# Kernel optimization log

Hardware: AMD Instinct MI355X
Metric: run time of the kernel (lower is better)

Reference implementation:

```python
import jax, jax.numpy as jnp
import numpy as np

GROUP_DIMS = (128, 64, 128, 64)  # per-group feature widths, sum = 384
ATTN_OUT = 64                    # per-group attention output width
B, W = 65536, 3                  # batch, words (4 groups * 3 words * 64 = 768 = linear_inner in-features)


def setup_inputs() -> dict:
    key = jax.random.key(0)
    keys = iter(jax.random.split(key, 64))
    s = 0.02
    inp = {"words": jax.random.normal(next(keys), (B, W, sum(GROUP_DIMS)), jnp.float32)}
    for g, d in enumerate(GROUP_DIMS):
        inp[f"wqkv{g}"] = jax.random.normal(next(keys), (d, 3 * d), jnp.float32) * s
        inp[f"bqkv{g}"] = jnp.zeros((3 * d,), jnp.float32)
        inp[f"wo{g}"] = jax.random.normal(next(keys), (d, ATTN_OUT), jnp.float32) * s
        inp[f"bo{g}"] = jnp.zeros((ATTN_OUT,), jnp.float32)
    inp["wi"] = jax.random.normal(next(keys), (ATTN_OUT * 12, 256), jnp.float32) * s
    inp["bi"] = jnp.zeros((256,), jnp.float32)
    inp["wout"] = jax.random.normal(next(keys), (256, 1), jnp.float32) * s
    inp["bout"] = jnp.zeros((1,), jnp.float32)
    return inp


def _group_attn(x, wqkv, bqkv, wo, bo, d):
    # x: [B, W, d] -> self-attention over W words within this feature group
    qkv = x @ wqkv + bqkv                      # [B, W, 3d]
    q, k, v = jnp.split(qkv, 3, axis=-1)       # each [B, W, d]
    scores = jnp.einsum('bqd,bkd->bqk', q, k) / jnp.sqrt(jnp.float32(d))
    attn = jax.nn.softmax(scores, axis=-1)     # [B, W, W]
    out = jnp.einsum('bqk,bkd->bqd', attn, v)  # [B, W, d]
    return out @ wo + bo                       # [B, W, ATTN_OUT]


def reference(words, wqkv0, bqkv0, wo0, bo0, wqkv1, bqkv1, wo1, bo1,
              wqkv2, bqkv2, wo2, bo2, wqkv3, bqkv3, wo3, bo3,
              wi, bi, wout, bout):
    gp = [(wqkv0, bqkv0, wo0, bo0), (wqkv1, bqkv1, wo1, bo1),
          (wqkv2, bqkv2, wo2, bo2), (wqkv3, bqkv3, wo3, bo3)]
    outs, start = [], 0
    for (wqkv, bqkv, wo, bo), d in zip(gp, GROUP_DIMS):
        outs.append(_group_attn(words[..., start:start + d], wqkv, bqkv, wo, bo, d))
        start += d
    cat = jnp.concatenate(outs, axis=-2)                 # [B, 12, 64]
    flat = jax.nn.relu(cat.reshape(cat.shape[0], -1))    # [B, 768]
    inner = jax.nn.relu(flat @ wi + bi)                  # [B, 256]
    return inner @ wout + bout                           # [B, 1]
```

## Files before the change

### kernel.cpp

```cpp
#include <hip/hip_runtime.h>

typedef _Float16 f16;
typedef _Float16 half8 __attribute__((ext_vector_type(8)));
typedef _Float16 half4 __attribute__((ext_vector_type(4)));
typedef float f32x4 __attribute__((ext_vector_type(4)));

#define BTOT 65536

static const size_t OFF_FLAT = 0;
static const size_t SZ_FLAT  = (size_t)BTOT * 768 * 2;
static const size_t OFF_WIT  = OFF_FLAT + SZ_FLAT;
static const size_t SZ_WIT   = (size_t)256 * 768 * 2;
static const size_t SZ_WT128 = (size_t)208 * 128 * 2;
static const size_t SZ_WT64  = (size_t)144 * 64 * 2;
static const size_t OFF_WT0  = OFF_WIT + SZ_WIT;
static const size_t OFF_WT1  = OFF_WT0 + SZ_WT128;
static const size_t OFF_WT2  = OFF_WT1 + SZ_WT64;
static const size_t OFF_WT3  = OFF_WT2 + SZ_WT128;
static const size_t OFF_CO   = OFF_WT3 + SZ_WT64;
static const size_t OFF_C    = OFF_CO + 256 * 4;

__global__ __launch_bounds__(256) void pk_fuse(
    const float* __restrict__ wq0, const float* __restrict__ bq0, const float* __restrict__ wo0, const float* __restrict__ bo0,
    const float* __restrict__ wq1, const float* __restrict__ bq1, const float* __restrict__ wo1, const float* __restrict__ bo1,
    const float* __restrict__ wq2, const float* __restrict__ bq2, const float* __restrict__ wo2, const float* __restrict__ bo2,
    const float* __restrict__ wq3, const float* __restrict__ bq3, const float* __restrict__ wo3, const float* __restrict__ bo3,
    f16* __restrict__ wT0, f16* __restrict__ wT1, f16* __restrict__ wT2, f16* __restrict__ wT3,
    float* __restrict__ coAll, float* __restrict__ cAll)
{
    const int g = blockIdx.y;
    const float* wqkv; const float* bqkv; const float* wo; const float* bo; f16* wT; int D;
    switch (g) {
        case 0:  wqkv = wq0; bqkv = bq0; wo = wo0; bo = bo0; wT = wT0; D = 128; break;
        case 1:  wqkv = wq1; bqkv = bq1; wo = wo1; bo = bo1; wT = wT1; D = 64;  break;
        case 2:  wqkv = wq2; bqkv = bq2; wo = wo2; bo = bo2; wT = wT2; D = 128; break;
        default: wqkv = wq3; bqkv = bq3; wo = wo3; bo = bo3; wT = wT3; D = 64;  break;
    }
    const int sh = (D == 128) ? 7 : 6;
    const int NT = (D + 81) / 16;
    const int NTD = (NT * 16) << sh;
    const int total = NTD + 65;
    const int o = blockIdx.x * 256 + threadIdx.x;
    if (o >= total) return;
    const int s3 = 3 * D;
    const float sc = rsqrtf((float)D);
    if (o < NTD) {
        const int n = o >> sh, k = o & (D - 1);
        float val = 0.f;
        if (n < D) {
            const float* a = wqkv + (size_t)k * s3;
            const float* b = wqkv + (size_t)n * s3 + D;
            float s = 0.f;
            for (int m = 0; m < D; ++m) s += a[m] * b[m];
            val = s * sc;
        } else if (n < D + 64) {
            const int j = n - D;
            const float* a = wqkv + (size_t)k * s3 + 2 * D;
            float s = 0.f;
            for (int m = 0; m < D; ++m) s += a[m] * wo[m * 64 + j];
            val = s;
        } else if (n == D + 64) {
            const float* a = wqkv + (size_t)k * s3;
            float s = 0.f;
            for (int m = 0; m < D; ++m) s += a[m] * bqkv[D + m];
            val = s * sc;
        } else if (n == D + 65) {
            const float* a = wqkv + (size_t)k * s3 + D;
            float s = 0.f;
            for (int m = 0; m < D; ++m) s += a[m] * bqkv[m];
            val = s * sc;
        }
        wT[o] = (f16)val;
    } else if (o < NTD + 64) {
        const int j = o - NTD;
        float s = 0.f;
        for (int m = 0; m < D; ++m) s += bqkv[2 * D + m] * wo[m * 64 + j];
        coAll[g * 64 + j] = s + bo[j];
    } else {
        float s = 0.f;
        for (int m = 0; m < D; ++m) s += bqkv[m] * bqkv[D + m];
        cAll[g] = s * sc;
    }
}

__global__ __launch_bounds__(256) void pk_wit(const float* __restrict__ wi, f16* __restrict__ wiT)
{
    int o = blockIdx.x * 256 + threadIdx.x;
    int n = o / 768, k = o - n * 768;
    wiT[o] = (f16)wi[k * 256 + n];
}

template<int D>
__device__ __forceinline__ void do_group(
    const float* __restrict__ words, const f16* __restrict__ wT,
    const float* __restrict__ co_g, const float* __restrict__ cAll, int gidx,
    f16* __restrict__ flat, int b0, int start, int gbase, int t, char* smem)
{
    constexpr int KST = D / 32;
    constexpr int NT  = (D + 81) / 16;
    constexpr int XP  = D + 8;
    constexpr int F4  = D / 4;
    constexpr int NLD = 48 * F4 / 256;

    f16 (*Xs)[XP]   = (f16(*)[XP])(smem);
    f16 (*Zs)[XP]   = (f16(*)[XP])(smem + (size_t)48 * XP * 2);
    f16 (*Zvo)[72]  = (f16(*)[72])(smem + (size_t)96 * XP * 2);
    float* Sc       = (float*)(smem + (size_t)96 * XP * 2 + 48 * 72 * 2);
    float (*xuw)[2] = (float(*)[2])(Sc + 144);

    const int wc = t >> 6, lane = t & 63;
    const int lrow = lane & 15, lk = lane >> 4;

    {
        float4 v[NLD];
        const int r0 = t / F4, c4 = t - r0 * F4;
        #pragma unroll
        for (int i = 0; i < NLD; ++i) {
            int r = r0 + i * (256 / F4);
            v[i] = *(const float4*)&words[(size_t)(b0 * 3 + r) * 384 + start + c4 * 4];
        }
        #pragma unroll
        for (int i = 0; i < NLD; ++i) {
            int r = r0 + i * (256 / F4);
            half4 h; h[0] = (f16)v[i].x; h[1] = (f16)v[i].y; h[2] = (f16)v[i].z; h[3] = (f16)v[i].w;
            *(half4*)&Xs[r][c4 * 4] = h;
        }
    }
    __syncthreads();

    {
        f32x4 acc[3][4];
        #pragma unroll
        for (int rt = 0; rt < 3; ++rt)
            #pragma unroll
            for (int ci = 0; ci < 4; ++ci) acc[rt][ci] = f32x4{0.f, 0.f, 0.f, 0.f};

        const f16* wbase = wT + (size_t)lrow * D + lk * 8;
        half8 bA[4], bB[4];

#define LOADB(BUF, KK)                                                          \
        { _Pragma("unroll")                                                     \
          for (int ci = 0; ci < 4; ++ci) {                                      \
              int ct = wc + ci * 4;                                             \
              if (ct < NT) BUF[ci] = *(const half8*)&wbase[(size_t)ct * 16 * D + (KK) * 32]; \
          } }
#define MSTEP(BUF, KK)                                                          \
        { half8 a0 = *(const half8*)&Xs[ 0 + lrow][(KK) * 32 + lk * 8];         \
          half8 a1 = *(const half8*)&Xs[16 + lrow][(KK) * 32 + lk * 8];         \
          half8 a2 = *(const half8*)&Xs[32 + lrow][(KK) * 32 + lk * 8];         \
          _Pragma("unroll")                                                     \
          for (int ci = 0; ci < 4; ++ci) {                                      \
              int ct = wc + ci * 4;                                             \
              if (ct < NT) {                                                    \
                  acc[0][ci] = __builtin_amdgcn_mfma_f32_16x16x32_f16(a0, BUF[ci], acc[0][ci], 0, 0, 0); \
                  acc[1][ci] = __builtin_amdgcn_mfma_f32_16x16x32_f16(a1, BUF[ci], acc[1][ci], 0, 0, 0); \
                  acc[2][ci] = __builtin_amdgcn_mfma_f32_16x16x32_f16(a2, BUF[ci], acc[2][ci], 0, 0, 0); \
              } } }

        LOADB(bA, 0)
        #pragma unroll
        for (int kp = 0; kp < KST / 2; ++kp) {
            LOADB(bB, 2 * kp + 1)
            MSTEP(bA, 2 * kp)
            if (2 * kp + 2 < KST) LOADB(bA, 2 * kp + 2)
            MSTEP(bB, 2 * kp + 1)
        }
#undef LOADB
#undef MSTEP

        #pragma unroll
        for (int ci = 0; ci < 4; ++ci) {
            int ct = wc + ci * 4;
            if (ct >= NT) continue;
            int n0 = ct * 16;
            if (n0 + 16 <= D) {
                #pragma unroll
                for (int rt = 0; rt < 3; ++rt)
                    #pragma unroll
                    for (int r = 0; r < 4; ++r)
                        Zs[rt * 16 + lk * 4 + r][n0 + lrow] = (f16)acc[rt][ci][r];
            } else if (n0 < D + 64) {
                #pragma unroll
                for (int rt = 0; rt < 3; ++rt)
                    #pragma unroll
                    for (int r = 0; r < 4; ++r)
                        Zvo[rt * 16 + lk * 4 + r][n0 - D + lrow] = (f16)acc[rt][ci][r];
            } else {
                if (lrow < 2) {
                    #pragma unroll
                    for (int rt = 0; rt < 3; ++rt)
                        #pragma unroll
                        for (int r = 0; r < 4; ++r)
                            xuw[rt * 16 + lk * 4 + r][lrow] = acc[rt][ci][r];
                }
            }
        }
    }
    __syncthreads();

    {
        const float cval = cAll[gidx];
        #pragma unroll
        for (int j = 0; j < 3; ++j) {
            int tt = wc + j * 4;
            if (tt < 9) {
                int rt = tt / 3, ct = tt - rt * 3;
                f32x4 s = f32x4{0.f, 0.f, 0.f, 0.f};
                #pragma unroll
                for (int kk = 0; kk < KST; ++kk) {
                    half8 a = *(const half8*)&Zs[rt * 16 + lrow][kk * 32 + lk * 8];
                    half8 b = *(const half8*)&Xs[ct * 16 + lrow][kk * 32 + lk * 8];
                    s = __builtin_amdgcn_mfma_f32_16x16x32_f16(a, b, s, 0, 0, 0);
                }
                #pragma unroll
                for (int r = 0; r < 4; ++r) {
                    int r1 = rt * 16 + lk * 4 + r;
                    int r2 = ct * 16 + lrow;
                    int b1 = r1 / 3, w1 = r1 - b1 * 3;
                    int b2 = r2 / 3, w2 = r2 - b2 * 3;
                    if (b1 == b2)
                        Sc[b1 * 9 + w1 * 3 + w2] =
                            s[r] + xuw[r1][0] + xuw[r2][1] + cval;
                }
            }
        }
    }
    __syncthreads();

    for (int i = t; i < 384; i += 256) {
        int b = i / 24, rem = i - b * 24;
        int w1 = rem >> 3, c8 = rem & 7;
        float s0 = Sc[b * 9 + w1 * 3 + 0];
        float s1 = Sc[b * 9 + w1 * 3 + 1];
        float s2 = Sc[b * 9 + w1 * 3 + 2];
        float m = fmaxf(s0, fmaxf(s1, s2));
        float e0 = __expf(s0 - m), e1 = __expf(s1 - m), e2 = __expf(s2 - m);
        float inv = 1.0f / (e0 + e1 + e2);
        float4 cA4 = *(const float4*)&co_g[c8 * 8];
        float4 cB4 = *(const float4*)&co_g[c8 * 8 + 4];
        float cov[8] = {cA4.x, cA4.y, cA4.z, cA4.w, cB4.x, cB4.y, cB4.z, cB4.w};
        half8 z0 = *(const half8*)&Zvo[b * 3 + 0][c8 * 8];
        half8 z1 = *(const half8*)&Zvo[b * 3 + 1][c8 * 8];
        half8 z2 = *(const half8*)&Zvo[b * 3 + 2][c8 * 8];
        half8 o;
        #pragma unroll
        for (int jj = 0; jj < 8; ++jj) {
            float v = (e0 * (float)z0[jj] + e1 * (float)z1[jj] + e2 * (float)z2[jj]) * inv
                      + cov[jj];
            o[jj] = (f16)fmaxf(v, 0.f);
        }
        *(half8*)&flat[(size_t)(b0 + b) * 768 + gbase + w1 * 64 + c8 * 8] = o;
    }
}

__global__ __launch_bounds__(256, 4) void k1(
    const float* __restrict__ words,
    const f16* __restrict__ wT0, const f16* __restrict__ wT1,
    const f16* __restrict__ wT2, const f16* __restrict__ wT3,
    const float* __restrict__ coAll, const float* __restrict__ cAll,
    f16* __restrict__ flat)
{
    extern __shared__ char smem[];
    const int t = threadIdx.x;
    const int b0 = blockIdx.x * 16;
    const int g = blockIdx.y;
    if (g == 0)
        do_group<128>(words, wT0, coAll + 0,   cAll, 0, flat, b0, 0,   0,   t, smem);
    else if (g == 1)
        do_group<64> (words, wT1, coAll + 64,  cAll, 1, flat, b0, 128, 192, t, smem);
    else if (g == 2)
        do_group<128>(words, wT2, coAll + 128, cAll, 2, flat, b0, 192, 384, t, smem);
    else
        do_group<64> (words, wT3, coAll + 192, cAll, 3, flat, b0, 320, 576, t, smem);
}

__global__ __launch_bounds__(512, 4) void k2_mlp(
    const f16* __restrict__ flat, const f16* __restrict__ wiT,
    const float* __restrict__ bi, const float* __restrict__ wout, const float* __restrict__ bout,
    float* __restrict__ out)
{
    __shared__ f16 Wsh[256][72];
    __shared__ float part[128][2];
    __shared__ float bi_l[256], wo_l[256];

    const int t = threadIdx.x;
    const int b0 = blockIdx.x * 128;
    if (t < 256) { bi_l[t] = bi[t]; wo_l[t] = wout[t]; }

    const int wv = t >> 6, lane = t & 63;
    const int wr = wv >> 1, wc = wv & 1;
    const int lrow = lane & 15, lk = lane >> 4;

    const int pn = t >> 3, pc8 = t & 7;
    half8 wreg[4];
    #pragma unroll
    for (int j = 0; j < 4; ++j)
        wreg[j] = *(const half8*)&wiT[(size_t)(pn + j * 64) * 768 + pc8 * 8];

    const f16* arow0 = flat + (size_t)(b0 + wr * 32 + lrow) * 768;
    const f16* arow1 = flat + (size_t)(b0 + wr * 32 + 16 + lrow) * 768;

    f32x4 acc[2][8];
    #pragma unroll
    for (int i = 0; i < 2; ++i)
        #pragma unroll
        for (int j = 0; j < 8; ++j) acc[i][j] = f32x4{0.f, 0.f, 0.f, 0.f};

    for (int kc = 0; kc < 12; ++kc) {
        #pragma unroll
        for (int j = 0; j < 4; ++j)
            *(half8*)&Wsh[pn + j * 64][pc8 * 8] = wreg[j];
        __syncthreads();
        if (kc + 1 < 12) {
            #pragma unroll
            for (int j = 0; j < 4; ++j)
                wreg[j] = *(const half8*)&wiT[(size_t)(pn + j * 64) * 768 + (kc + 1) * 64 + pc8 * 8];
        }
        #pragma unroll
        for (int ks = 0; ks < 2; ++ks) {
            half8 a0 = *(const half8*)&arow0[kc * 64 + ks * 32 + lk * 8];
            half8 a1 = *(const half8*)&arow1[kc * 64 + ks * 32 + lk * 8];
            #pragma unroll
            for (int ct = 0; ct < 8; ++ct) {
                half8 b = *(const half8*)&Wsh[wc * 128 + ct * 16 + lrow][ks * 32 + lk * 8];
                acc[0][ct] = __builtin_amdgcn_mfma_f32_16x16x32_f16(a0, b, acc[0][ct], 0, 0, 0);
                acc[1][ct] = __builtin_amdgcn_mfma_f32_16x16x32_f16(a1, b, acc[1][ct], 0, 0, 0);
            }
        }
        __syncthreads();
    }

    float bo0 = bout[0];
    #pragma unroll
    for (int rt = 0; rt < 2; ++rt) {
        #pragma unroll
        for (int r = 0; r < 4; ++r) {
            float s = 0.f;
            #pragma unroll
            for (int ct = 0; ct < 8; ++ct) {
                int col = wc * 128 + ct * 16 + lrow;
                float v = acc[rt][ct][r] + bi_l[col];
                v = fmaxf(v, 0.f);
                s += v * wo_l[col];
            }
            s += __shfl_xor(s, 1, 64); s += __shfl_xor(s, 2, 64);
            s += __shfl_xor(s, 4, 64); s += __shfl_xor(s, 8, 64);
            if (lrow == 0) part[wr * 32 + rt * 16 + lk * 4 + r][wc] = s;
        }
    }
    __syncthreads();
    if (t < 128) out[b0 + t] = part[t][0] + part[t][1] + bo0;
}

extern "C" void kernel_launch(void* const* d_in, const int* in_sizes, int n_in,
                              void* d_out, int out_size, void* d_ws, size_t ws_size,
                              hipStream_t stream)
{
    const float* words = (const float*)d_in[0];
    const float* wq[4] = {(const float*)d_in[1], (const float*)d_in[5], (const float*)d_in[9],  (const float*)d_in[13]};
    const float* bq[4] = {(const float*)d_in[2], (const float*)d_in[6], (const float*)d_in[10], (const float*)d_in[14]};
    const float* wo[4] = {(const float*)d_in[3], (const float*)d_in[7], (const float*)d_in[11], (const float*)d_in[15]};
    const float* bo[4] = {(const float*)d_in[4], (const float*)d_in[8], (const float*)d_in[12], (const float*)d_in[16]};
    const float* wi   = (const float*)d_in[17];
    const float* bi   = (const float*)d_in[18];
    const float* wout = (const float*)d_in[19];
    const float* bout = (const float*)d_in[20];

    char* ws = (char*)d_ws;
    f16*   flat = (f16*)(ws + OFF_FLAT);
    f16*   wiT  = (f16*)(ws + OFF_WIT);
    f16*   wT0  = (f16*)(ws + OFF_WT0);
    f16*   wT1  = (f16*)(ws + OFF_WT1);
    f16*   wT2  = (f16*)(ws + OFF_WT2);
    f16*   wT3  = (f16*)(ws + OFF_WT3);
    float* coA  = (float*)(ws + OFF_CO);
    float* cA   = (float*)(ws + OFF_C);

    pk_fuse<<<dim3(105, 4), 256, 0, stream>>>(
        wq[0], bq[0], wo[0], bo[0], wq[1], bq[1], wo[1], bo[1],
        wq[2], bq[2], wo[2], bo[2], wq[3], bq[3], wo[3], bo[3],
        wT0, wT1, wT2, wT3, coA, cA);
    pk_wit<<<768, 256, 0, stream>>>(wi, wiT);

    k1<<<dim3(4096, 4), 256, 34304, stream>>>(words, wT0, wT1, wT2, wT3, coA, cA, flat);

    k2_mlp<<<512, 512, 0, stream>>>(flat, wiT, bi, wout, bout, (float*)d_out);
}
```

Before: 238.1 us.

## Make attention kernel persistent with register prefetch and retile the MLP kernel

The attention kernel becomes a persistent grid of 1280 blocks. Each block loops over 16-batch tiles of one feature group and prefetches the next tile's words into registers while the current tile runs its MFMA work, so global-load latency overlaps compute. Shared memory shrinks by packing the score and xu/xw scratch into the row padding, which lets the occupancy hint rise to 5 blocks. It also switches to a packed fp16 convert (round-toward-zero) and hoists the bias vector loads out of the loop. The MLP kernel is retiled to 64 rows per block with four column warps, doubling its grid, at the cost of reloading the weight tiles twice as often.

```diff
diff --git a/kernel.cpp b/kernel.cpp
--- a/kernel.cpp
+++ b/kernel.cpp
@@ -3,6 +3,7 @@
 typedef _Float16 f16;
 typedef _Float16 half8 __attribute__((ext_vector_type(8)));
 typedef _Float16 half4 __attribute__((ext_vector_type(4)));
+typedef __fp16 fp16x2 __attribute__((ext_vector_type(2)));
 typedef float f32x4 __attribute__((ext_vector_type(4)));
 
 #define BTOT 65536
@@ -19,6 +20,15 @@
 static const size_t OFF_WT3  = OFF_WT2 + SZ_WT128;
 static const size_t OFF_CO   = OFF_WT3 + SZ_WT64;
 static const size_t OFF_C    = OFF_CO + 256 * 4;
+
+__device__ __forceinline__ half4 cvt4(float4 v) {
+    fp16x2 lo = __builtin_amdgcn_cvt_pkrtz(v.x, v.y);
+    fp16x2 hi = __builtin_amdgcn_cvt_pkrtz(v.z, v.w);
+    half4 h;
+    h[0] = (_Float16)lo[0]; h[1] = (_Float16)lo[1];
+    h[2] = (_Float16)hi[0]; h[3] = (_Float16)hi[1];
+    return h;
+}
 
 __global__ __launch_bounds__(256) void pk_fuse(
     const float* __restrict__ wq0, const float* __restrict__ bq0, const float* __restrict__ wo0, const float* __restrict__ bo0,
@@ -91,169 +101,190 @@
 }
 
 template<int D>
-__device__ __forceinline__ void do_group(
+__device__ __forceinline__ void run_group(
     const float* __restrict__ words, const f16* __restrict__ wT,
-    const float* __restrict__ co_g, const float* __restrict__ cAll, int gidx,
-    f16* __restrict__ flat, int b0, int start, int gbase, int t, char* smem)
+    const float* __restrict__ coAll, const float* __restrict__ cAll, int gidx,
+    f16* __restrict__ flat, int x0, int GX, int start, int gbase, int t, char* smem)
 {
     constexpr int KST = D / 32;
     constexpr int NT  = (D + 81) / 16;
     constexpr int XP  = D + 8;
     constexpr int F4  = D / 4;
     constexpr int NLD = 48 * F4 / 256;
-
-    f16 (*Xs)[XP]   = (f16(*)[XP])(smem);
-    f16 (*Zs)[XP]   = (f16(*)[XP])(smem + (size_t)48 * XP * 2);
-    f16 (*Zvo)[72]  = (f16(*)[72])(smem + (size_t)96 * XP * 2);
-    float* Sc       = (float*)(smem + (size_t)96 * XP * 2 + 48 * 72 * 2);
-    float (*xuw)[2] = (float(*)[2])(Sc + 144);
+    const int NX = 4096;
+
+    f16 (*Xs)[XP]  = (f16(*)[XP])(smem);
+    f16 (*Zs)[XP]  = (f16(*)[XP])(smem + (size_t)48 * XP * 2);
+    f16 (*Zvo)[64] = (f16(*)[64])(smem + (size_t)96 * XP * 2);
 
     const int wc = t >> 6, lane = t & 63;
     const int lrow = lane & 15, lk = lane >> 4;
-
+    const int r0 = t / F4, c4 = t - r0 * F4;
+
+    const float cval = cAll[gidx];
+    float cov[8];
     {
-        float4 v[NLD];
-        const int r0 = t / F4, c4 = t - r0 * F4;
+        const int c8 = t & 7;
+        float4 cA4 = *(const float4*)&coAll[gidx * 64 + c8 * 8];
+        float4 cB4 = *(const float4*)&coAll[gidx * 64 + c8 * 8 + 4];
+        cov[0]=cA4.x; cov[1]=cA4.y; cov[2]=cA4.z; cov[3]=cA4.w;
+        cov[4]=cB4.x; cov[5]=cB4.y; cov[6]=cB4.z; cov[7]=cB4.w;
+    }
+    const f16* wbase = wT + (size_t)lrow * D + lk * 8;
+
+    float4 pre[NLD];
+    {
+        int b0 = x0 * 16;
         #pragma unroll
         for (int i = 0; i < NLD; ++i) {
             int r = r0 + i * (256 / F4);
-            v[i] = *(const float4*)&words[(size_t)(b0 * 3 + r) * 384 + start + c4 * 4];
-        }
+            pre[i] = *(const float4*)&words[(size_t)(b0 * 3 + r) * 384 + start + c4 * 4];
+        }
+    }
+
+    for (int tile = x0; tile < NX; tile += GX) {
+        const int b0 = tile * 16;
+
         #pragma unroll
         for (int i = 0; i < NLD; ++i) {
             int r = r0 + i * (256 / F4);
-            half4 h; h[0] = (f16)v[i].x; h[1] = (f16)v[i].y; h[2] = (f16)v[i].z; h[3] = (f16)v[i].w;
-            *(half4*)&Xs[r][c4 * 4] = h;
-        }
-    }
-    __syncthreads();
-
-    {
-        f32x4 acc[3][4];
-        #pragma unroll
-        for (int rt = 0; rt < 3; ++rt)
-            #pragma unroll
-            for (int ci = 0; ci < 4; ++ci) acc[rt][ci] = f32x4{0.f, 0.f, 0.f, 0.f};
-
-        const f16* wbase = wT + (size_t)lrow * D + lk * 8;
-        half8 bA[4], bB[4];
+            *(half4*)&Xs[r][c4 * 4] = cvt4(pre[i]);
+        }
+        __syncthreads();
+
+        {
+            int nt = (tile + GX < NX) ? (tile + GX) : tile;
+            int nb0 = nt * 16;
+            #pragma unroll
+            for (int i = 0; i < NLD; ++i) {
+                int r = r0 + i * (256 / F4);
+                pre[i] = *(const float4*)&words[(size_t)(nb0 * 3 + r) * 384 + start + c4 * 4];
+            }
+        }
+
+        {
+            f32x4 acc[3][4];
+            #pragma unroll
+            for (int rt = 0; rt < 3; ++rt)
+                #pragma unroll
+                for (int ci = 0; ci < 4; ++ci) acc[rt][ci] = f32x4{0.f, 0.f, 0.f, 0.f};
+
+            half8 bA[4], bB[4];
 
 #define LOADB(BUF, KK)                                                          \
-        { _Pragma("unroll")                                                     \
-          for (int ci = 0; ci < 4; ++ci) {                                      \
-              int ct = wc + ci * 4;                                             \
-              if (ct < NT) BUF[ci] = *(const half8*)&wbase[(size_t)ct * 16 * D + (KK) * 32]; \
-          } }
+            { _Pragma("unroll")                                                 \
+              for (int ci = 0; ci < 4; ++ci) {                                  \
+                  int ct = wc + ci * 4;                                         \
+                  if (ct < NT) BUF[ci] = *(const half8*)&wbase[(size_t)ct * 16 * D + (KK) * 32]; \
+              } }
 #define MSTEP(BUF, KK)                                                          \
-        { half8 a0 = *(const half8*)&Xs[ 0 + lrow][(KK) * 32 + lk * 8];         \
-          half8 a1 = *(const half8*)&Xs[16 + lrow][(KK) * 32 + lk * 8];         \
-          half8 a2 = *(const half8*)&Xs[32 + lrow][(KK) * 32 + lk * 8];         \
-          _Pragma("unroll")                                                     \
-          for (int ci = 0; ci < 4; ++ci) {                                      \
-              int ct = wc + ci * 4;                                             \
-              if (ct < NT) {                                                    \
-                  acc[0][ci] = __builtin_amdgcn_mfma_f32_16x16x32_f16(a0, BUF[ci], acc[0][ci], 0, 0, 0); \
-                  acc[1][ci] = __builtin_amdgcn_mfma_f32_16x16x32_f16(a1, BUF[ci], acc[1][ci], 0, 0, 0); \
-                  acc[2][ci] = __builtin_amdgcn_mfma_f32_16x16x32_f16(a2, BUF[ci], acc[2][ci], 0, 0, 0); \
-              } } }
-
-        LOADB(bA, 0)
-        #pragma unroll
-        for (int kp = 0; kp < KST / 2; ++kp) {
-            LOADB(bB, 2 * kp + 1)
-            MSTEP(bA, 2 * kp)
-            if (2 * kp + 2 < KST) LOADB(bA, 2 * kp + 2)
-            MSTEP(bB, 2 * kp + 1)
-        }
+            { half8 a0 = *(const half8*)&Xs[ 0 + lrow][(KK) * 32 + lk * 8];     \
+              half8 a1 = *(const half8*)&Xs[16 + lrow][(KK) * 32 + lk * 8];     \
+              half8 a2 = *(const half8*)&Xs[32 + lrow][(KK) * 32 + lk * 8];     \
+              _Pragma("unroll")                                                 \
+              for (int ci = 0; ci < 4; ++ci) {                                  \
+                  int ct = wc + ci * 4;                                         \
+                  if (ct < NT) {                                                \
+                      acc[0][ci] = __builtin_amdgcn_mfma_f32_16x16x32_f16(a0, BUF[ci], acc[0][ci], 0, 0, 0); \
+                      acc[1][ci] = __builtin_amdgcn_mfma_f32_16x16x32_f16(a1, BUF[ci], acc[1][ci], 0, 0, 0); \
+                      acc[2][ci] = __builtin_amdgcn_mfma_f32_16x16x32_f16(a2, BUF[ci], acc[2][ci], 0, 0, 0); \
+                  } } }
+
+            LOADB(bA, 0)
+            #pragma unroll
+            for (int kp = 0; kp < KST / 2; ++kp) {
+                LOADB(bB, 2 * kp + 1)
+                MSTEP(bA, 2 * kp)
+                if (2 * kp + 2 < KST) LOADB(bA, 2 * kp + 2)
+                MSTEP(bB, 2 * kp + 1)
+            }
 #undef LOADB
 #undef MSTEP
 
-        #pragma unroll
-        for (int ci = 0; ci < 4; ++ci) {
-            int ct = wc + ci * 4;
-            if (ct >= NT) continue;
-            int n0 = ct * 16;
-            if (n0 + 16 <= D) {
-                #pragma unroll
-                for (int rt = 0; rt < 3; ++rt)
-                    #pragma unroll
-                    for (int r = 0; r < 4; ++r)
-                        Zs[rt * 16 + lk * 4 + r][n0 + lrow] = (f16)acc[rt][ci][r];
-            } else if (n0 < D + 64) {
-                #pragma unroll
-                for (int rt = 0; rt < 3; ++rt)
-                    #pragma unroll
-                    for (int r = 0; r < 4; ++r)
-                        Zvo[rt * 16 + lk * 4 + r][n0 - D + lrow] = (f16)acc[rt][ci][r];
-            } else {
-                if (lrow < 2) {
+            #pragma unroll
+            for (int ci = 0; ci < 4; ++ci) {
+                int ct = wc + ci * 4;
+                if (ct >= NT) continue;
+                int n0 = ct * 16;
+                if (n0 + 16 <= D) {
                     #pragma unroll
                     for (int rt = 0; rt < 3; ++rt)
                         #pragma unroll
                         for (int r = 0; r < 4; ++r)
-                            xuw[rt * 16 + lk * 4 + r][lrow] = acc[rt][ci][r];
+                            Zs[rt * 16 + lk * 4 + r][n0 + lrow] = (f16)acc[rt][ci][r];
+                } else if (n0 < D + 64) {
+                    #pragma unroll
+                    for (int rt = 0; rt < 3; ++rt)
+                        #pragma unroll
+                        for (int r = 0; r < 4; ++r)
+                            Zvo[rt * 16 + lk * 4 + r][n0 - D + lrow] = (f16)acc[rt][ci][r];
+                } else {
+                    if (lrow < 2) {
+                        #pragma unroll
+                        for (int rt = 0; rt < 3; ++rt)
+                            #pragma unroll
+                            for (int r = 0; r < 4; ++r)
+                                ((float*)((char*)&Zs[rt * 16 + lk * 4 + r][D]))[lrow] = acc[rt][ci][r];
+                    }
                 }
             }
         }
-    }
-    __syncthreads();
-
-    {
-        const float cval = cAll[gidx];
-        #pragma unroll
-        for (int j = 0; j < 3; ++j) {
-            int tt = wc + j * 4;
-            if (tt < 9) {
-                int rt = tt / 3, ct = tt - rt * 3;
-                f32x4 s = f32x4{0.f, 0.f, 0.f, 0.f};
-                #pragma unroll
-                for (int kk = 0; kk < KST; ++kk) {
-                    half8 a = *(const half8*)&Zs[rt * 16 + lrow][kk * 32 + lk * 8];
-                    half8 b = *(const half8*)&Xs[ct * 16 + lrow][kk * 32 + lk * 8];
-                    s = __builtin_amdgcn_mfma_f32_16x16x32_f16(a, b, s, 0, 0, 0);
+        __syncthreads();
+
+        {
+            #pragma unroll
+            for (int j = 0; j < 3; ++j) {
+                int tt = wc + j * 4;
+                if (tt < 9) {
+                    int rt = tt / 3, ct = tt - rt * 3;
+                    f32x4 s = f32x4{0.f, 0.f, 0.f, 0.f};
+                    #pragma unroll
+                    for (int kk = 0; kk < KST; ++kk) {
+                        half8 a = *(const half8*)&Zs[rt * 16 + lrow][kk * 32 + lk * 8];
+                        half8 b = *(const half8*)&Xs[ct * 16 + lrow][kk * 32 + lk * 8];
+                        s = __builtin_amdgcn_mfma_f32_16x16x32_f16(a, b, s, 0, 0, 0);
+                    }
+                    #pragma unroll
+                    for (int r = 0; r < 4; ++r) {
+                        int r1 = rt * 16 + lk * 4 + r;
+                        int r2 = ct * 16 + lrow;
+                        int b1 = r1 / 3, w1 = r1 - b1 * 3;
+                        int b2 = r2 / 3, w2 = r2 - b2 * 3;
+                        if (b1 == b2) {
+                            float xu = ((const float*)((const char*)&Zs[r1][D]))[0];
+                            float xw = ((const float*)((const char*)&Zs[r2][D]))[1];
+                            ((float*)((char*)&Xs[b1 * 3 + w1][D]))[w2] = s[r] + xu + xw + cval;
+                        }
+                    }
                 }
-                #pragma unroll
-                for (int r = 0; r < 4; ++r) {
-                    int r1 = rt * 16 + lk * 4 + r;
-                    int r2 = ct * 16 + lrow;
-                    int b1 = r1 / 3, w1 = r1 - b1 * 3;
-                    int b2 = r2 / 3, w2 = r2 - b2 * 3;
-                    if (b1 == b2)
-                        Sc[b1 * 9 + w1 * 3 + w2] =
-                            s[r] + xuw[r1][0] + xuw[r2][1] + cval;
-                }
-            }
-        }
-    }
-    __syncthreads();
-
-    for (int i = t; i < 384; i += 256) {
-        int b = i / 24, rem = i - b * 24;
-        int w1 = rem >> 3, c8 = rem & 7;
-        float s0 = Sc[b * 9 + w1 * 3 + 0];
-        float s1 = Sc[b * 9 + w1 * 3 + 1];
-        float s2 = Sc[b * 9 + w1 * 3 + 2];
-        float m = fmaxf(s0, fmaxf(s1, s2));
-        float e0 = __expf(s0 - m), e1 = __expf(s1 - m), e2 = __expf(s2 - m);
-        float inv = 1.0f / (e0 + e1 + e2);
-        float4 cA4 = *(const float4*)&co_g[c8 * 8];
-        float4 cB4 = *(const float4*)&co_g[c8 * 8 + 4];
-        float cov[8] = {cA4.x, cA4.y, cA4.z, cA4.w, cB4.x, cB4.y, cB4.z, cB4.w};
-        half8 z0 = *(const half8*)&Zvo[b * 3 + 0][c8 * 8];
-        half8 z1 = *(const half8*)&Zvo[b * 3 + 1][c8 * 8];
-        half8 z2 = *(const half8*)&Zvo[b * 3 + 2][c8 * 8];
-        half8 o;
-        #pragma unroll
-        for (int jj = 0; jj < 8; ++jj) {
-            float v = (e0 * (float)z0[jj] + e1 * (float)z1[jj] + e2 * (float)z2[jj]) * inv
-                      + cov[jj];
-            o[jj] = (f16)fmaxf(v, 0.f);
-        }
-        *(half8*)&flat[(size_t)(b0 + b) * 768 + gbase + w1 * 64 + c8 * 8] = o;
-    }
-}
-
-__global__ __launch_bounds__(256, 4) void k1(
+            }
+        }
+        __syncthreads();
+
+        for (int i = t; i < 384; i += 256) {
+            int b = i / 24, rem = i - b * 24;
+            int w1 = rem >> 3, c8 = rem & 7;
+            const float* sp = (const float*)((const char*)&Xs[b * 3 + w1][D]);
+            float s0 = sp[0], s1 = sp[1], s2 = sp[2];
+            float m = fmaxf(s0, fmaxf(s1, s2));
+            float e0 = __expf(s0 - m), e1 = __expf(s1 - m), e2 = __expf(s2 - m);
+            float inv = 1.0f / (e0 + e1 + e2);
+            half8 z0 = *(const half8*)&Zvo[b * 3 + 0][c8 * 8];
+            half8 z1 = *(const half8*)&Zvo[b * 3 + 1][c8 * 8];
+            half8 z2 = *(const half8*)&Zvo[b * 3 + 2][c8 * 8];
+            half8 o;
+            #pragma unroll
+            for (int jj = 0; jj < 8; ++jj) {
+                float v = (e0 * (float)z0[jj] + e1 * (float)z1[jj] + e2 * (float)z2[jj]) * inv
+                          + cov[jj];
+                o[jj] = (f16)fmaxf(v, 0.f);
+            }
+            *(half8*)&flat[(size_t)(b0 + b) * 768 + gbase + w1 * 64 + c8 * 8] = o;
+        }
+    }
+}
+
+__global__ __launch_bounds__(256, 5) void k1(
     const float* __restrict__ words,
     const f16* __restrict__ wT0, const f16* __restrict__ wT1,
     const f16* __restrict__ wT2, const f16* __restrict__ wT3,
@@ -262,33 +293,34 @@
 {
     extern __shared__ char smem[];
     const int t = threadIdx.x;
-    const int b0 = blockIdx.x * 16;
-    const int g = blockIdx.y;
+    const int g  = blockIdx.x & 3;
+    const int x0 = blockIdx.x >> 2;
+    const int GX = gridDim.x >> 2;
     if (g == 0)
-        do_group<128>(words, wT0, coAll + 0,   cAll, 0, flat, b0, 0,   0,   t, smem);
+        run_group<128>(words, wT0, coAll, cAll, 0, flat, x0, GX, 0,   0,   t, smem);
     else if (g == 1)
-        do_group<64> (words, wT1, coAll + 64,  cAll, 1, flat, b0, 128, 192, t, smem);
+        run_group<64> (words, wT1, coAll, cAll, 1, flat, x0, GX, 128, 192, t, smem);
     else if (g == 2)
-        do_group<128>(words, wT2, coAll + 128, cAll, 2, flat, b0, 192, 384, t, smem);
+        run_group<128>(words, wT2, coAll, cAll, 2, flat, x0, GX, 192, 384, t, smem);
     else
-        do_group<64> (words, wT3, coAll + 192, cAll, 3, flat, b0, 320, 576, t, smem);
-}
-
-__global__ __launch_bounds__(512, 4) void k2_mlp(
+        run_group<64> (words, wT3, coAll, cAll, 3, flat, x0, GX, 320, 576, t, smem);
+}
+
+__global__ __launch_bounds__(512) void k2_mlp(
     const f16* __restrict__ flat, const f16* __restrict__ wiT,
     const float* __restrict__ bi, const float* __restrict__ wout, const float* __restrict__ bout,
     float* __restrict__ out)
 {
     __shared__ f16 Wsh[256][72];
-    __shared__ float part[128][2];
+    __shared__ float part[64][4];
     __shared__ float bi_l[256], wo_l[256];
 
     const int t = threadIdx.x;
-    const int b0 = blockIdx.x * 128;
+    const int b0 = blockIdx.x * 64;
     if (t < 256) { bi_l[t] = bi[t]; wo_l[t] = wout[t]; }
 
     const int wv = t >> 6, lane = t & 63;
-    const int wr = wv >> 1, wc = wv & 1;
+    const int wr = wv >> 2, wc = wv & 3;
     const int lrow = lane & 15, lk = lane >> 4;
 
     const int pn = t >> 3, pc8 = t & 7;
@@ -300,11 +332,11 @@
     const f16* arow0 = flat + (size_t)(b0 + wr * 32 + lrow) * 768;
     const f16* arow1 = flat + (size_t)(b0 + wr * 32 + 16 + lrow) * 768;
 
-    f32x4 acc[2][8];
+    f32x4 acc[2][4];
     #pragma unroll
     for (int i = 0; i < 2; ++i)
         #pragma unroll
-        for (int j = 0; j < 8; ++j) acc[i][j] = f32x4{0.f, 0.f, 0.f, 0.f};
+        for (int j = 0; j < 4; ++j) acc[i][j] = f32x4{0.f, 0.f, 0.f, 0.f};
 
     for (int kc = 0; kc < 12; ++kc) {
         #pragma unroll
@@ -321,8 +353,8 @@
             half8 a0 = *(const half8*)&arow0[kc * 64 + ks * 32 + lk * 8];
             half8 a1 = *(const half8*)&arow1[kc * 64 + ks * 32 + lk * 8];
             #pragma unroll
-            for (int ct = 0; ct < 8; ++ct) {
-                half8 b = *(const half8*)&Wsh[wc * 128 + ct * 16 + lrow][ks * 32 + lk * 8];
+            for (int ct = 0; ct < 4; ++ct) {
+                half8 b = *(const half8*)&Wsh[wc * 64 + ct * 16 + lrow][ks * 32 + lk * 8];
                 acc[0][ct] = __builtin_amdgcn_mfma_f32_16x16x32_f16(a0, b, acc[0][ct], 0, 0, 0);
                 acc[1][ct] = __builtin_amdgcn_mfma_f32_16x16x32_f16(a1, b, acc[1][ct], 0, 0, 0);
             }
@@ -337,8 +369,8 @@
         for (int r = 0; r < 4; ++r) {
             float s = 0.f;
             #pragma unroll
-            for (int ct = 0; ct < 8; ++ct) {
-                int col = wc * 128 + ct * 16 + lrow;
+            for (int ct = 0; ct < 4; ++ct) {
+                int col = wc * 64 + ct * 16 + lrow;
                 float v = acc[rt][ct][r] + bi_l[col];
                 v = fmaxf(v, 0.f);
                 s += v * wo_l[col];
@@ -349,7 +381,9 @@
         }
     }
     __syncthreads();
-    if (t < 128) out[b0 + t] = part[t][0] + part[t][1] + bo0;
+    if (t < 64) {
+        out[b0 + t] = part[t][0] + part[t][1] + part[t][2] + part[t][3] + bo0;
+    }
 }
 
 extern "C" void kernel_launch(void* const* d_in, const int* in_sizes, int n_in,
@@ -382,7 +416,7 @@
         wT0, wT1, wT2, wT3, coA, cA);
     pk_wit<<<768, 256, 0, stream>>>(wi, wiT);
 
-    k1<<<dim3(4096, 4), 256, 34304, stream>>>(words, wT0, wT1, wT2, wT3, coA, cA, flat);
-
-    k2_mlp<<<512, 512, 0, stream>>>(flat, wiT, bi, wout, bout, (float*)d_out);
-}
+    k1<<<1280, 256, 32256, stream>>>(words, wT0, wT1, wT2, wT3, coA, cA, flat);
+
+    k2_mlp<<<1024, 512, 0, stream>>>(flat, wiT, bi, wout, bout, (float*)d_out);
+}
```

After: 836.8 us. +251.5%, slower.
